# Optimization experiments

Hardware: AMD Instinct MI355X
Metric: run time of the kernel (lower is better)

The kernel has to match this reference:

```python
import jax, jax.numpy as jnp
import numpy as np

NUM_BINS = 16
D_MODEL = 128
TAIL_BOUND = 20.0
MIN_BIN_WIDTH = 1e-3
MIN_BIN_HEIGHT = 1e-3
MIN_DERIVATIVE = 1e-3
EPS = 1e-6


def setup_inputs() -> dict:
    key = jax.random.key(0)
    ks = jax.random.split(key, 10)
    B, S = 32, 8192
    sc = 0.05  # small init scale so spline logits stay moderate
    return {
        "inputs": jax.random.normal(ks[0], (B, S), dtype=jnp.float32),
        "conditioning": jax.random.normal(ks[1], (B, S, D_MODEL), dtype=jnp.float32),
        "Ww": jax.random.normal(ks[2], (NUM_BINS, D_MODEL), dtype=jnp.float32) * sc,
        "bw": jax.random.normal(ks[3], (NUM_BINS,), dtype=jnp.float32) * sc,
        "Wh": jax.random.normal(ks[4], (NUM_BINS, D_MODEL), dtype=jnp.float32) * sc,
        "bh": jax.random.normal(ks[5], (NUM_BINS,), dtype=jnp.float32) * sc,
        "Wd": jax.random.normal(ks[6], (NUM_BINS - 1, D_MODEL), dtype=jnp.float32) * sc,
        "bd": jax.random.normal(ks[7], (NUM_BINS - 1,), dtype=jnp.float32) * sc,
        "Wl": jax.random.normal(ks[8], (NUM_BINS, D_MODEL), dtype=jnp.float32) * sc,
        "bl": jax.random.normal(ks[9], (NUM_BINS,), dtype=jnp.float32) * sc,
    }


def _rational_linear_spline(x, uw, uh, ud, ul, left, right, bottom, top):
    nb = uw.shape[-1]
    # bin widths / cumulative widths
    w = MIN_BIN_WIDTH + (1.0 - MIN_BIN_WIDTH * nb) * jax.nn.softmax(uw, axis=-1)
    cw = jnp.concatenate([jnp.zeros_like(w[..., :1]), jnp.cumsum(w, axis=-1)], axis=-1)
    cw = (right - left) * cw + left
    cw = cw.at[..., 0].set(left).at[..., -1].set(right)
    w = cw[..., 1:] - cw[..., :-1]
    # derivatives (ud already padded to nb+1 by caller)
    d = MIN_DERIVATIVE + jax.nn.softplus(ud)
    # bin heights / cumulative heights
    h = MIN_BIN_HEIGHT + (1.0 - MIN_BIN_HEIGHT * nb) * jax.nn.softmax(uh, axis=-1)
    ch = jnp.concatenate([jnp.zeros_like(h[..., :1]), jnp.cumsum(h, axis=-1)], axis=-1)
    ch = (top - bottom) * ch + bottom
    ch = ch.at[..., 0].set(bottom).at[..., -1].set(top)
    h = ch[..., 1:] - ch[..., :-1]
    # searchsorted via sum of comparisons (as in source)
    locs = cw.at[..., -1].add(EPS)
    idx = jnp.sum((x[..., None] >= locs).astype(jnp.int32), axis=-1) - 1
    idx = jnp.clip(idx, 0, nb - 1)
    g = lambda t: jnp.take_along_axis(t, idx[..., None], axis=-1)[..., 0]
    in_cw = g(cw)
    in_bw = g(w)
    in_ch = g(ch)
    in_delta = g(h / w)
    dk = g(d)
    dk1 = g(d[..., 1:])
    in_h = g(h)
    lambdas = 0.95 * jax.nn.sigmoid(ul) + 0.025
    lam = g(lambdas)
    wa = 1.0
    wb = jnp.sqrt(dk / dk1) * wa
    wc = (lam * wa * dk + (1.0 - lam) * wb * dk1) / in_delta
    ya = in_ch
    yb = in_h + in_ch
    yc = ((1.0 - lam) * wa * ya + lam * wb * yb) / ((1.0 - lam) * wa + lam * wb)
    theta = (x - in_cw) / in_bw
    m = theta <= lam
    num = jnp.where(m, wa * ya * (lam - theta) + wc * yc * theta,
                    wc * yc * (1.0 - theta) + wb * yb * (theta - lam))
    den = jnp.where(m, wa * (lam - theta) + wc * theta,
                    wc * (1.0 - theta) + wb * (theta - lam))
    out = num / den
    deriv_num = jnp.where(m, wa * wc * lam * (yc - ya), wb * wc * (1.0 - lam) * (yb - yc)) / in_bw
    logabsdet = jnp.log(deriv_num) - 2.0 * jnp.log(jnp.abs(den))
    return out, logabsdet


def reference(inputs, conditioning, Ww, bw, Wh, bh, Wd, bd, Wl, bl):
    # parameter nets (module.forward): note the module normalizes here AND the
    # spline normalizes again -- replicate faithfully.
    uw = jax.nn.softmax(jnp.einsum('bsd,kd->bsk', conditioning, Ww) + bw, axis=-1)
    uh = jax.nn.softmax(jnp.einsum('bsd,kd->bsk', conditioning, Wh) + bh, axis=-1)
    ud = jax.nn.softplus(jnp.einsum('bsd,kd->bsk', conditioning, Wd) + bd)
    ul = jax.nn.sigmoid(jnp.einsum('bsd,kd->bsk', conditioning, Wl) + bl)
    # linear tails: pad derivatives with constant so boundary derivative == 1
    const = float(np.log(np.exp(1.0 - MIN_DERIVATIVE) - 1.0))
    edge = jnp.full(ud.shape[:-1] + (1,), const, dtype=ud.dtype)
    udp = jnp.concatenate([edge, ud, edge], axis=-1)  # [B,S,nb+1]
    tb = TAIL_BOUND
    inside = (inputs >= -tb) & (inputs <= tb)
    xc = jnp.clip(inputs, -tb, tb)
    s_out, s_lad = _rational_linear_spline(xc, uw, uh, udp, ul, -tb, tb, -tb, tb)
    outputs = jnp.where(inside, s_out, inputs)
    logabsdet = jnp.where(inside, s_lad, 0.0)
    return outputs, logabsdet
```

## Files before the change

### kernel.cpp

```cpp
#include <hip/hip_runtime.h>
#include <math.h>

#define NB 16
#define DM 128
#define BM 256
#define ZSTRIDE 68

typedef _Float16 half8  __attribute__((ext_vector_type(8)));
typedef _Float16 half4v __attribute__((ext_vector_type(4)));
typedef _Float16 half2v __attribute__((ext_vector_type(2)));
typedef __fp16   fp16x2 __attribute__((ext_vector_type(2)));
typedef float    f32x4  __attribute__((ext_vector_type(4)));

__device__ __forceinline__ float frcp_(float x) { return __builtin_amdgcn_rcpf(x); }
__device__ __forceinline__ float softplus_fast(float x) {
    return fmaxf(x, 0.0f) + __logf(1.0f + __expf(-fabsf(x)));
}
__device__ __forceinline__ float sigmoid_fast(float x) {
    return frcp_(1.0f + __expf(-x));
}
__device__ __forceinline__ void softmax16_m(float* z) {
    float m = z[0];
#pragma unroll
    for (int k = 1; k < NB; k++) m = fmaxf(m, z[k]);
    float s = 0.0f;
#pragma unroll
    for (int k = 0; k < NB; k++) { z[k] = __expf(z[k] - m); s += z[k]; }
    float r = frcp_(s);
#pragma unroll
    for (int k = 0; k < NB; k++) z[k] *= r;
}
__device__ __forceinline__ void softmax16_nm(float* z) {
    float s = 0.0f;
#pragma unroll
    for (int k = 0; k < NB; k++) { z[k] = __expf(z[k]); s += z[k]; }
    float r = frcp_(s);
#pragma unroll
    for (int k = 0; k < NB; k++) z[k] *= r;
}

__device__ __forceinline__ half2v pk_(float lo, float hi) {
    fp16x2 p = __builtin_amdgcn_cvt_pkrtz(lo, hi);
    return __builtin_bit_cast(half2v, p);
}
__device__ __forceinline__ half8 cvt8(float4 a0, float4 a1) {
    half2v p0 = pk_(a0.x, a0.y);
    half2v p1 = pk_(a0.z, a0.w);
    half2v p2 = pk_(a1.x, a1.y);
    half2v p3 = pk_(a1.z, a1.w);
    half8 f;
    f[0] = p0[0]; f[1] = p0[1]; f[2] = p1[0]; f[3] = p1[1];
    f[4] = p2[0]; f[5] = p2[1]; f[6] = p3[0]; f[7] = p3[1];
    return f;
}

#define LOADC(P, cr)                                    \
    P##0 = *(const float4*)((cr) + 0);                  \
    P##1 = *(const float4*)((cr) + 16);                 \
    P##2 = *(const float4*)((cr) + 32);                 \
    P##3 = *(const float4*)((cr) + 48);                 \
    P##4 = *(const float4*)((cr) + 64);                 \
    P##5 = *(const float4*)((cr) + 80);                 \
    P##6 = *(const float4*)((cr) + 96);                 \
    P##7 = *(const float4*)((cr) + 112);

#define CVTC(P)                                         \
    af0 = cvt8(P##0, P##1);                             \
    af1 = cvt8(P##2, P##3);                             \
    af2 = cvt8(P##4, P##5);                             \
    af3 = cvt8(P##6, P##7);

#define MFMA_S(af, s)                                                           \
    acc0 = __builtin_amdgcn_mfma_f32_16x16x32_f16(af, B0##s, acc0, 0, 0, 0);    \
    acc1 = __builtin_amdgcn_mfma_f32_16x16x32_f16(af, B1##s, acc1, 0, 0, 0);    \
    acc2 = __builtin_amdgcn_mfma_f32_16x16x32_f16(af, B2##s, acc2, 0, 0, 0);    \
    acc3 = __builtin_amdgcn_mfma_f32_16x16x32_f16(af, B3##s, acc3, 0, 0, 0);

#define STOREZ(c) {                                                             \
    _Float16* zpw = zbase + (size_t)((c) * 16) * ZSTRIDE;                       \
    _Pragma("unroll")                                                           \
    for (int r = 0; r < 4; r++) {                                               \
        half2v p0 = pk_(acc0[r], acc1[r]);                                      \
        half2v p1 = pk_(acc2[r], acc3[r]);                                      \
        half4v w; w[0] = p0[0]; w[1] = p0[1]; w[2] = p1[0]; w[3] = p1[1];       \
        *(half4v*)(zpw + (size_t)r * ZSTRIDE) = w;                              \
    } }

#define RESET_ACC  acc0 = zf4; acc1 = zf4; acc2 = zf4; acc3 = zf4;

#define GEMM_CHUNK(P, c)                                                        \
    CVTC(P)                                                                     \
    MFMA_S(af0, 0) MFMA_S(af1, 1) MFMA_S(af2, 2) MFMA_S(af3, 3)                 \
    STOREZ(c) RESET_ACC

#define STAGE_B(Wt, isWd, Q0, Q1, Q2, Q3) {                                     \
    const bool val = (!(isWd)) || (l15 < 15);                                   \
    const float* srcl = (Wt) + (size_t)(val ? l15 : 0) * DM + lg * 4;           \
    float4 q0 = *(const float4*)(srcl + 0),  q1 = *(const float4*)(srcl + 16);  \
    float4 q2 = *(const float4*)(srcl + 32), q3 = *(const float4*)(srcl + 48);  \
    float4 q4 = *(const float4*)(srcl + 64), q5 = *(const float4*)(srcl + 80);  \
    float4 q6 = *(const float4*)(srcl + 96), q7 = *(const float4*)(srcl + 112); \
    Q0 = val ? cvt8(q0, q1) : hz;                                               \
    Q1 = val ? cvt8(q2, q3) : hz;                                               \
    Q2 = val ? cvt8(q4, q5) : hz;                                               \
    Q3 = val ? cvt8(q6, q7) : hz; }

#define FENCE_LDS                                       \
    __builtin_amdgcn_sched_barrier(0);                  \
    asm volatile("s_waitcnt lgkmcnt(0)" ::: "memory");  \
    __builtin_amdgcn_sched_barrier(0);

#define EPILOGUE(xv, giv)                                                        \
  if ((giv) < (size_t)N) {                                                       \
    float zw[NB], zh[NB], zl[NB], zd[NB - 1];                                    \
    const half4v* zr4 = (const half4v*)&Z[(size_t)tid * ZSTRIDE];                \
    _Pragma("unroll")                                                            \
    for (int j = 0; j < NB; j++) {                                               \
        half4v v = zr4[j];                                                       \
        zw[j] = (float)v[0] + bw[j];                                             \
        zh[j] = (float)v[1] + bh[j];                                             \
        zl[j] = (float)v[2] + bl[j];                                             \
        if (j < NB - 1) zd[j] = (float)v[3] + bd[j];                             \
    }                                                                            \
    float xc = fminf(fmaxf((xv), -20.0f), 20.0f);                                \
    softmax16_m(zw);                                                             \
    softmax16_nm(zw);                                                            \
    const float scale = (1.0f - 1e-3f * NB);                                     \
    float cw[NB + 1];                                                            \
    cw[0] = -20.0f;                                                              \
    float cum = 0.0f;                                                            \
    _Pragma("unroll")                                                            \
    for (int k = 0; k < NB; k++) {                                               \
        cum += 1e-3f + scale * zw[k];                                            \
        cw[k + 1] = 40.0f * cum - 20.0f;                                         \
    }                                                                            \
    cw[NB] = 20.0f;                                                              \
    softmax16_m(zh);                                                             \
    softmax16_nm(zh);                                                            \
    float ch[NB + 1];                                                            \
    ch[0] = -20.0f;                                                              \
    cum = 0.0f;                                                                  \
    _Pragma("unroll")                                                            \
    for (int k = 0; k < NB; k++) {                                               \
        cum += 1e-3f + scale * zh[k];                                            \
        ch[k + 1] = 40.0f * cum - 20.0f;                                         \
    }                                                                            \
    ch[NB] = 20.0f;                                                              \
    float in_cw = cw[0], cw_hi = cw[1], in_ch = ch[0], ch_hi = ch[1];            \
    float zl_sel = zl[0], zd_lo = zd[0], zd_hi = zd[0];                          \
    _Pragma("unroll")                                                            \
    for (int k = 1; k < NB; k++) {                                               \
        bool take = (xc >= cw[k]);                                               \
        in_cw  = take ? cw[k]     : in_cw;                                       \
        cw_hi  = take ? cw[k + 1] : cw_hi;                                       \
        in_ch  = take ? ch[k]     : in_ch;                                       \
        ch_hi  = take ? ch[k + 1] : ch_hi;                                       \
        zl_sel = take ? zl[k]     : zl_sel;                                      \
        zd_lo  = take ? zd[k - 1] : zd_lo;                                       \
        zd_hi  = take ? zd[(k < NB - 1) ? k : NB - 2] : zd_hi;                   \
    }                                                                            \
    bool firstbin = (xc <  cw[1]);                                               \
    bool lastbin  = (xc >= cw[NB - 1]);                                          \
    float in_bw = cw_hi - in_cw;                                                 \
    float in_h  = ch_hi - in_ch;                                                 \
    float dk  = firstbin ? 1.0f : (1e-3f + softplus_fast(softplus_fast(zd_lo))); \
    float dk1 = lastbin  ? 1.0f : (1e-3f + softplus_fast(softplus_fast(zd_hi))); \
    float ul  = sigmoid_fast(zl_sel);                                            \
    float lam = 0.95f * sigmoid_fast(ul) + 0.025f;                               \
    float rbw = frcp_(in_bw);                                                    \
    float in_delta = in_h * rbw;                                                 \
    float wb = sqrtf(dk * frcp_(dk1));                                           \
    float wc = (lam * dk + (1.0f - lam) * wb * dk1) * frcp_(in_delta);           \
    float ya = in_ch;                                                            \
    float yb = in_h + in_ch;                                                     \
    float yc = ((1.0f - lam) * ya + lam * wb * yb) * frcp_((1.0f - lam) + lam * wb); \
    float theta = (xc - in_cw) * rbw;                                            \
    bool mlt = (theta <= lam);                                                   \
    float num = mlt ? (ya * (lam - theta) + wc * yc * theta)                     \
                    : (wc * yc * (1.0f - theta) + wb * yb * (theta - lam));      \
    float den = mlt ? ((lam - theta) + wc * theta)                               \
                    : (wc * (1.0f - theta) + wb * (theta - lam));                \
    float sout = num * frcp_(den);                                               \
    float dnum = (mlt ? (wc * lam * (yc - ya))                                   \
                      : (wb * wc * (1.0f - lam) * (yb - yc))) * rbw;             \
    float slad = __logf(dnum) - 2.0f * __logf(fabsf(den));                       \
    bool inside = ((xv) >= -20.0f) && ((xv) <= 20.0f);                           \
    out[(giv)] = inside ? sout : (xv);                                           \
    lad[(giv)] = inside ? slad : 0.0f;                                           \
  }

__global__ __launch_bounds__(256, 2) void spline_mfma(
    const float* __restrict__ xin, const float* __restrict__ cond,
    const float* __restrict__ Ww, const float* __restrict__ bw,
    const float* __restrict__ Wh, const float* __restrict__ bh,
    const float* __restrict__ Wd, const float* __restrict__ bd,
    const float* __restrict__ Wl, const float* __restrict__ bl,
    float* __restrict__ out, float* __restrict__ lad, int N)
{
    __shared__ __align__(16) _Float16 Z[BM * ZSTRIDE];

    const int tid  = threadIdx.x;
    const int wave = tid >> 6;
    const int lane = tid & 63;
    const int l15  = lane & 15;
    const int lg   = lane >> 4;

    const int nTiles = (N + BM - 1) / BM;
    const int t0 = (int)blockIdx.x;
    const int t1 = t0 + (int)gridDim.x;
    const bool hasT1 = (t1 < nTiles);

    half8 hz;
    hz[0]=hz[1]=hz[2]=hz[3]=hz[4]=hz[5]=hz[6]=hz[7] = (_Float16)0.0f;
    half8 B00, B01, B02, B03, B10, B11, B12, B13,
          B20, B21, B22, B23, B30, B31, B32, B33;
    STAGE_B(Ww, false, B00, B01, B02, B03)
    STAGE_B(Wh, false, B10, B11, B12, B13)
    STAGE_B(Wl, false, B20, B21, B22, B23)
    STAGE_B(Wd, true,  B30, B31, B32, B33)

    const size_t bRow0 = (size_t)t0 * BM;
    const size_t gi0 = bRow0 + tid;
    size_t g00 = bRow0 + (size_t)(wave * 64 + l15);
    size_t g01 = g00 + 16, g02 = g00 + 32, g03 = g00 + 48;
    if (g00 >= (size_t)N) g00 = (size_t)N - 1;
    if (g01 >= (size_t)N) g01 = (size_t)N - 1;
    if (g02 >= (size_t)N) g02 = (size_t)N - 1;
    if (g03 >= (size_t)N) g03 = (size_t)N - 1;

    float4 A0_0, A0_1, A0_2, A0_3, A0_4, A0_5, A0_6, A0_7;
    float4 A1_0, A1_1, A1_2, A1_3, A1_4, A1_5, A1_6, A1_7;
    float4 A2_0, A2_1, A2_2, A2_3, A2_4, A2_5, A2_6, A2_7;
    float4 A3_0, A3_1, A3_2, A3_3, A3_4, A3_5, A3_6, A3_7;
    LOADC(A0_, cond + g00 * DM + lg * 4)
    LOADC(A1_, cond + g01 * DM + lg * 4)
    LOADC(A2_, cond + g02 * DM + lg * 4)
    LOADC(A3_, cond + g03 * DM + lg * 4)
    float x0 = xin[gi0 < (size_t)N ? gi0 : 0];

    const f32x4 zf4 = {0.f, 0.f, 0.f, 0.f};
    f32x4 acc0 = zf4, acc1 = zf4, acc2 = zf4, acc3 = zf4;
    half8 af0, af1, af2, af3;
    _Float16* zbase = &Z[(size_t)(wave * 64 + lg * 4) * ZSTRIDE + l15 * 4];

    GEMM_CHUNK(A0_, 0)
    GEMM_CHUNK(A1_, 1)
    GEMM_CHUNK(A2_, 2)
    GEMM_CHUNK(A3_, 3)

    const size_t bRow1 = (size_t)t1 * BM;
    const size_t gi1 = bRow1 + tid;
    size_t g10 = bRow1 + (size_t)(wave * 64 + l15);
    size_t g11 = g10 + 16, g12 = g10 + 32, g13 = g10 + 48;
    if (g10 >= (size_t)N) g10 = (size_t)N - 1;
    if (g11 >= (size_t)N) g11 = (size_t)N - 1;
    if (g12 >= (size_t)N) g12 = (size_t)N - 1;
    if (g13 >= (size_t)N) g13 = (size_t)N - 1;
    float x1 = 0.0f;
    if (hasT1) {
        LOADC(A0_, cond + g10 * DM + lg * 4)
        LOADC(A1_, cond + g11 * DM + lg * 4)
        x1 = xin[gi1 < (size_t)N ? gi1 : 0];
    }

    FENCE_LDS
    EPILOGUE(x0, gi0)

    if (hasT1) {
        LOADC(A2_, cond + g12 * DM + lg * 4)
        LOADC(A3_, cond + g13 * DM + lg * 4)
        GEMM_CHUNK(A0_, 0)
        GEMM_CHUNK(A1_, 1)
        GEMM_CHUNK(A2_, 2)
        GEMM_CHUNK(A3_, 3)
        FENCE_LDS
        EPILOGUE(x1, gi1)
    }
}

extern "C" void kernel_launch(void* const* d_in, const int* in_sizes, int n_in,
                              void* d_out, int out_size, void* d_ws, size_t ws_size,
                              hipStream_t stream) {
    const float* xin  = (const float*)d_in[0];
    const float* cond = (const float*)d_in[1];
    const float* Ww   = (const float*)d_in[2];
    const float* bwp  = (const float*)d_in[3];
    const float* Wh   = (const float*)d_in[4];
    const float* bhp  = (const float*)d_in[5];
    const float* Wd   = (const float*)d_in[6];
    const float* bdp  = (const float*)d_in[7];
    const float* Wl   = (const float*)d_in[8];
    const float* blp  = (const float*)d_in[9];
    int N = in_sizes[0];
    float* out = (float*)d_out;
    float* lad = out + N;
    int nTiles = (N + BM - 1) / BM;
    int grid = (nTiles + 1) / 2;
    hipLaunchKernelGGL(spline_mfma, dim3(grid), dim3(256), 0, stream,
                       xin, cond, Ww, bwp, Wh, bhp, Wd, bdp, Wl, blp, out, lad, N);
}
```

Baseline: 35.29 us.

## Rotate three conditioning register buffers and compute spline knots inside the bin search

The prefetch schedule now rotates three A-register buffer sets instead of four. Loads for later chunks and the next tile are issued right after the buffer they reuse has been consumed by the MFMA chunk. The epilogue also computes cumulative widths and heights on the fly inside the bin-selection loop instead of materialising the cw/ch arrays. Together these lower register pressure, which could help occupancy, but they leave less prefetch distance before each chunk's data is needed.

```diff
diff --git a/kernel.cpp b/kernel.cpp
--- a/kernel.cpp
+++ b/kernel.cpp
@@ -109,6 +109,10 @@
     __builtin_amdgcn_sched_barrier(0);                  \
     asm volatile("s_waitcnt lgkmcnt(0)" ::: "memory");  \
     __builtin_amdgcn_sched_barrier(0);
+
+#define CPTR(t, c) (cond + ((((size_t)(t) * BM + (size_t)(wave * 64 + (c) * 16 + l15)) < (size_t)N) \
+                    ? ((size_t)(t) * BM + (size_t)(wave * 64 + (c) * 16 + l15))                     \
+                    : ((size_t)N - 1)) * DM + lg * 4)
 
 #define EPILOGUE(xv, giv)                                                        \
   if ((giv) < (size_t)N) {                                                       \
@@ -123,44 +127,35 @@
         if (j < NB - 1) zd[j] = (float)v[3] + bd[j];                             \
     }                                                                            \
     float xc = fminf(fmaxf((xv), -20.0f), 20.0f);                                \
-    softmax16_m(zw);                                                             \
-    softmax16_nm(zw);                                                            \
+    softmax16_m(zw); softmax16_nm(zw);                                           \
+    softmax16_m(zh); softmax16_nm(zh);                                           \
     const float scale = (1.0f - 1e-3f * NB);                                     \
-    float cw[NB + 1];                                                            \
-    cw[0] = -20.0f;                                                              \
-    float cum = 0.0f;                                                            \
-    _Pragma("unroll")                                                            \
-    for (int k = 0; k < NB; k++) {                                               \
-        cum += 1e-3f + scale * zw[k];                                            \
-        cw[k + 1] = 40.0f * cum - 20.0f;                                         \
-    }                                                                            \
-    cw[NB] = 20.0f;                                                              \
-    softmax16_m(zh);                                                             \
-    softmax16_nm(zh);                                                            \
-    float ch[NB + 1];                                                            \
-    ch[0] = -20.0f;                                                              \
-    cum = 0.0f;                                                                  \
-    _Pragma("unroll")                                                            \
-    for (int k = 0; k < NB; k++) {                                               \
-        cum += 1e-3f + scale * zh[k];                                            \
-        ch[k + 1] = 40.0f * cum - 20.0f;                                         \
-    }                                                                            \
-    ch[NB] = 20.0f;                                                              \
-    float in_cw = cw[0], cw_hi = cw[1], in_ch = ch[0], ch_hi = ch[1];            \
+    float cum_w = 1e-3f + scale * zw[0];                                         \
+    float cum_h = 1e-3f + scale * zh[0];                                         \
+    float cw_k1 = 40.0f * cum_w - 20.0f;                              \
+    float ch_k1 = 40.0f * cum_h - 20.0f;                                         \
+    const float cw1 = cw_k1;                                                     \
+    float in_cw = -20.0f, cw_hi = cw_k1, in_ch = -20.0f, ch_hi = ch_k1;          \
     float zl_sel = zl[0], zd_lo = zd[0], zd_hi = zd[0];                          \
+    bool lastbin = false;                                                        \
     _Pragma("unroll")                                                            \
     for (int k = 1; k < NB; k++) {                                               \
-        bool take = (xc >= cw[k]);                                               \
-        in_cw  = take ? cw[k]     : in_cw;                                       \
-        cw_hi  = take ? cw[k + 1] : cw_hi;                                       \
-        in_ch  = take ? ch[k]     : in_ch;                                       \
-        ch_hi  = take ? ch[k + 1] : ch_hi;                                       \
-        zl_sel = take ? zl[k]     : zl_sel;                                      \
+        cum_w += 1e-3f + scale * zw[k];                                          \
+        cum_h += 1e-3f + scale * zh[k];                                          \
+        float cw_k2 = (k == NB - 1) ? 20.0f : (40.0f * cum_w - 20.0f);           \
+        float ch_k2 = (k == NB - 1) ? 20.0f : (40.0f * cum_h - 20.0f);           \
+        bool take = (xc >= cw_k1);                              \
+        in_cw  = take ? cw_k1 : in_cw;                                           \
+        cw_hi  = take ? cw_k2 : cw_hi;                                           \
+        in_ch  = take ? ch_k1 : in_ch;                                           \
+        ch_hi  = take ? ch_k2 : ch_hi;                                           \
+        zl_sel = take ? zl[k] : zl_sel;                                          \
         zd_lo  = take ? zd[k - 1] : zd_lo;                                       \
         zd_hi  = take ? zd[(k < NB - 1) ? k : NB - 2] : zd_hi;                   \
+        if (k == NB - 1) lastbin = take;                                         \
+        cw_k1 = cw_k2; ch_k1 = ch_k2;                                            \
     }                                                                            \
-    bool firstbin = (xc <  cw[1]);                                               \
-    bool lastbin  = (xc >= cw[NB - 1]);                                          \
+    bool firstbin = (xc < cw1);                                                  \
     float in_bw = cw_hi - in_cw;                                                 \
     float in_h  = ch_hi - in_ch;                                                 \
     float dk  = firstbin ? 1.0f : (1e-3f + softplus_fast(softplus_fast(zd_lo))); \
@@ -219,23 +214,15 @@
     STAGE_B(Wl, false, B20, B21, B22, B23)
     STAGE_B(Wd, true,  B30, B31, B32, B33)
 
-    const size_t bRow0 = (size_t)t0 * BM;
-    const size_t gi0 = bRow0 + tid;
-    size_t g00 = bRow0 + (size_t)(wave * 64 + l15);
-    size_t g01 = g00 + 16, g02 = g00 + 32, g03 = g00 + 48;
-    if (g00 >= (size_t)N) g00 = (size_t)N - 1;
-    if (g01 >= (size_t)N) g01 = (size_t)N - 1;
-    if (g02 >= (size_t)N) g02 = (size_t)N - 1;
-    if (g03 >= (size_t)N) g03 = (size_t)N - 1;
+    const size_t gi0 = (size_t)t0 * BM + tid;
+    const size_t gi1 = (size_t)t1 * BM + tid;
 
     float4 A0_0, A0_1, A0_2, A0_3, A0_4, A0_5, A0_6, A0_7;
     float4 A1_0, A1_1, A1_2, A1_3, A1_4, A1_5, A1_6, A1_7;
     float4 A2_0, A2_1, A2_2, A2_3, A2_4, A2_5, A2_6, A2_7;
-    float4 A3_0, A3_1, A3_2, A3_3, A3_4, A3_5, A3_6, A3_7;
-    LOADC(A0_, cond + g00 * DM + lg * 4)
-    LOADC(A1_, cond + g01 * DM + lg * 4)
-    LOADC(A2_, cond + g02 * DM + lg * 4)
-    LOADC(A3_, cond + g03 * DM + lg * 4)
+    LOADC(A0_, CPTR(t0, 0))
+    LOADC(A1_, CPTR(t0, 1))
+    LOADC(A2_, CPTR(t0, 2))
     float x0 = xin[gi0 < (size_t)N ? gi0 : 0];
 
     const f32x4 zf4 = {0.f, 0.f, 0.f, 0.f};
@@ -244,22 +231,15 @@
     _Float16* zbase = &Z[(size_t)(wave * 64 + lg * 4) * ZSTRIDE + l15 * 4];
 
     GEMM_CHUNK(A0_, 0)
+    LOADC(A0_, CPTR(t0, 3))
     GEMM_CHUNK(A1_, 1)
+    float x1 = 0.0f;
+    if (hasT1) { LOADC(A1_, CPTR(t1, 0)) }
     GEMM_CHUNK(A2_, 2)
-    GEMM_CHUNK(A3_, 3)
-
-    const size_t bRow1 = (size_t)t1 * BM;
-    const size_t gi1 = bRow1 + tid;
-    size_t g10 = bRow1 + (size_t)(wave * 64 + l15);
-    size_t g11 = g10 + 16, g12 = g10 + 32, g13 = g10 + 48;
-    if (g10 >= (size_t)N) g10 = (size_t)N - 1;
-    if (g11 >= (size_t)N) g11 = (size_t)N - 1;
-    if (g12 >= (size_t)N) g12 = (size_t)N - 1;
-    if (g13 >= (size_t)N) g13 = (size_t)N - 1;
-    float x1 = 0.0f;
+    if (hasT1) { LOADC(A2_, CPTR(t1, 1)) }
+    GEMM_CHUNK(A0_, 3)
     if (hasT1) {
-        LOADC(A0_, cond + g10 * DM + lg * 4)
-        LOADC(A1_, cond + g11 * DM + lg * 4)
+        LOADC(A0_, CPTR(t1, 2))
         x1 = xin[gi1 < (size_t)N ? gi1 : 0];
     }
 
@@ -267,12 +247,11 @@
     EPILOGUE(x0, gi0)
 
     if (hasT1) {
-        LOADC(A2_, cond + g12 * DM + lg * 4)
-        LOADC(A3_, cond + g13 * DM + lg * 4)
-        GEMM_CHUNK(A0_, 0)
-        GEMM_CHUNK(A1_, 1)
-        GEMM_CHUNK(A2_, 2)
-        GEMM_CHUNK(A3_, 3)
+        GEMM_CHUNK(A1_, 0)
+        LOADC(A1_, CPTR(t1, 3))
+        GEMM_CHUNK(A2_, 1)
+        GEMM_CHUNK(A0_, 2)
+        GEMM_CHUNK(A1_, 3)
         FENCE_LDS
         EPILOGUE(x1, gi1)
     }
```

Measured after the change: 38.14 us. +8.1%, slower.

## Stage weights in LDS, process one tile per block, double-buffer loads

Applied to the files above, without the earlier changes.

Moves the converted fp16 weight fragments from per-thread registers into shared LDS, with each wave staging one weight matrix and then a block barrier. Each block now handles a single 256-row tile instead of two, and the conditioning loads use two rotating register buffers instead of four. Launch bounds rise to 3 blocks per CU. The aim is lower register pressure and higher occupancy, so that more memory requests are in flight. In exchange it adds LDS reads before every MFMA group, a __syncthreads, and repeats the weight staging in twice as many blocks.

```diff
diff --git a/kernel.cpp b/kernel.cpp
--- a/kernel.cpp
+++ b/kernel.cpp
@@ -70,11 +70,16 @@
     af2 = cvt8(P##4, P##5);                             \
     af3 = cvt8(P##6, P##7);
 
-#define MFMA_S(af, s)                                                           \
-    acc0 = __builtin_amdgcn_mfma_f32_16x16x32_f16(af, B0##s, acc0, 0, 0, 0);    \
-    acc1 = __builtin_amdgcn_mfma_f32_16x16x32_f16(af, B1##s, acc1, 0, 0, 0);    \
-    acc2 = __builtin_amdgcn_mfma_f32_16x16x32_f16(af, B2##s, acc2, 0, 0, 0);    \
-    acc3 = __builtin_amdgcn_mfma_f32_16x16x32_f16(af, B3##s, acc3, 0, 0, 0);
+#define MFMA_GRP(af, s) {                                                       \
+    const half8 bt0 = *(const half8*)(Blds + (((0*4+(s))*64 + lane) * 8));      \
+    const half8 bt1 = *(const half8*)(Blds + (((1*4+(s))*64 + lane) * 8));      \
+    const half8 bt2 = *(const half8*)(Blds + (((2*4+(s))*64 + lane) * 8));      \
+    const half8 bt3 = *(const half8*)(Blds + (((3*4+(s))*64 + lane) * 8));      \
+    acc0 = __builtin_amdgcn_mfma_f32_16x16x32_f16(af, bt0, acc0, 0, 0, 0);      \
+    acc1 = __builtin_amdgcn_mfma_f32_16x16x32_f16(af, bt1, acc1, 0, 0, 0);      \
+    acc2 = __builtin_amdgcn_mfma_f32_16x16x32_f16(af, bt2, acc2, 0, 0, 0);      \
+    acc3 = __builtin_amdgcn_mfma_f32_16x16x32_f16(af, bt3, acc3, 0, 0, 0);      \
+}
 
 #define STOREZ(c) {                                                             \
     _Float16* zpw = zbase + (size_t)((c) * 16) * ZSTRIDE;                       \
@@ -90,25 +95,34 @@
 
 #define GEMM_CHUNK(P, c)                                                        \
     CVTC(P)                                                                     \
-    MFMA_S(af0, 0) MFMA_S(af1, 1) MFMA_S(af2, 2) MFMA_S(af3, 3)                 \
+    MFMA_GRP(af0, 0) MFMA_GRP(af1, 1) MFMA_GRP(af2, 2) MFMA_GRP(af3, 3)         \
     STOREZ(c) RESET_ACC
 
-#define STAGE_B(Wt, isWd, Q0, Q1, Q2, Q3) {                                     \
+#define STAGE_B_LDS(Wt, isWd) {                                                 \
     const bool val = (!(isWd)) || (l15 < 15);                                   \
     const float* srcl = (Wt) + (size_t)(val ? l15 : 0) * DM + lg * 4;           \
     float4 q0 = *(const float4*)(srcl + 0),  q1 = *(const float4*)(srcl + 16);  \
     float4 q2 = *(const float4*)(srcl + 32), q3 = *(const float4*)(srcl + 48);  \
     float4 q4 = *(const float4*)(srcl + 64), q5 = *(const float4*)(srcl + 80);  \
     float4 q6 = *(const float4*)(srcl + 96), q7 = *(const float4*)(srcl + 112); \
-    Q0 = val ? cvt8(q0, q1) : hz;                                               \
-    Q1 = val ? cvt8(q2, q3) : hz;                                               \
-    Q2 = val ? cvt8(q4, q5) : hz;                                               \
-    Q3 = val ? cvt8(q6, q7) : hz; }
+    half8 Q0 = val ? cvt8(q0, q1) : hz;                                         \
+    half8 Q1 = val ? cvt8(q2, q3) : hz;                                         \
+    half8 Q2 = val ? cvt8(q4, q5) : hz;                                         \
+    half8 Q3 = val ? cvt8(q6, q7) : hz;                                         \
+    *(half8*)(Blds + (((wave*4+0)*64 + lane) * 8)) = Q0;                        \
+    *(half8*)(Blds + (((wave*4+1)*64 + lane) * 8)) = Q1;                        \
+    *(half8*)(Blds + (((wave*4+2)*64 + lane) * 8)) = Q2;                        \
+    *(half8*)(Blds + (((wave*4+3)*64 + lane) * 8)) = Q3;                        \
+}
 
 #define FENCE_LDS                                       \
     __builtin_amdgcn_sched_barrier(0);                  \
     asm volatile("s_waitcnt lgkmcnt(0)" ::: "memory");  \
     __builtin_amdgcn_sched_barrier(0);
+
+#define CPTR(c) (cond + (((bRow + (size_t)(wave * 64 + (c) * 16 + l15)) < (size_t)N) \
+                    ? (bRow + (size_t)(wave * 64 + (c) * 16 + l15))                  \
+                    : ((size_t)N - 1)) * DM + lg * 4)
 
 #define EPILOGUE(xv, giv)                                                        \
   if ((giv) < (size_t)N) {                                                       \
@@ -189,7 +203,7 @@
     lad[(giv)] = inside ? slad : 0.0f;                                           \
   }
 
-__global__ __launch_bounds__(256, 2) void spline_mfma(
+__global__ __launch_bounds__(256, 3) void spline_mfma(
     const float* __restrict__ xin, const float* __restrict__ cond,
     const float* __restrict__ Ww, const float* __restrict__ bw,
     const float* __restrict__ Wh, const float* __restrict__ bh,
@@ -198,6 +212,7 @@
     float* __restrict__ out, float* __restrict__ lad, int N)
 {
     __shared__ __align__(16) _Float16 Z[BM * ZSTRIDE];
+    __shared__ __align__(16) _Float16 Blds[16 * 64 * 8];
 
     const int tid  = threadIdx.x;
     const int wave = tid >> 6;
@@ -205,77 +220,38 @@
     const int l15  = lane & 15;
     const int lg   = lane >> 4;
 
-    const int nTiles = (N + BM - 1) / BM;
-    const int t0 = (int)blockIdx.x;
-    const int t1 = t0 + (int)gridDim.x;
-    const bool hasT1 = (t1 < nTiles);
+    const size_t bRow = (size_t)blockIdx.x * BM;
+    const size_t gi = bRow + tid;
 
     half8 hz;
     hz[0]=hz[1]=hz[2]=hz[3]=hz[4]=hz[5]=hz[6]=hz[7] = (_Float16)0.0f;
-    half8 B00, B01, B02, B03, B10, B11, B12, B13,
-          B20, B21, B22, B23, B30, B31, B32, B33;
-    STAGE_B(Ww, false, B00, B01, B02, B03)
-    STAGE_B(Wh, false, B10, B11, B12, B13)
-    STAGE_B(Wl, false, B20, B21, B22, B23)
-    STAGE_B(Wd, true,  B30, B31, B32, B33)
-
-    const size_t bRow0 = (size_t)t0 * BM;
-    const size_t gi0 = bRow0 + tid;
-    size_t g00 = bRow0 + (size_t)(wave * 64 + l15);
-    size_t g01 = g00 + 16, g02 = g00 + 32, g03 = g00 + 48;
-    if (g00 >= (size_t)N) g00 = (size_t)N - 1;
-    if (g01 >= (size_t)N) g01 = (size_t)N - 1;
-    if (g02 >= (size_t)N) g02 = (size_t)N - 1;
-    if (g03 >= (size_t)N) g03 = (size_t)N - 1;
-
-    float4 A0_0, A0_1, A0_2, A0_3, A0_4, A0_5, A0_6, A0_7;
-    float4 A1_0, A1_1, A1_2, A1_3, A1_4, A1_5, A1_6, A1_7;
-    float4 A2_0, A2_1, A2_2, A2_3, A2_4, A2_5, A2_6, A2_7;
-    float4 A3_0, A3_1, A3_2, A3_3, A3_4, A3_5, A3_6, A3_7;
-    LOADC(A0_, cond + g00 * DM + lg * 4)
-    LOADC(A1_, cond + g01 * DM + lg * 4)
-    LOADC(A2_, cond + g02 * DM + lg * 4)
-    LOADC(A3_, cond + g03 * DM + lg * 4)
-    float x0 = xin[gi0 < (size_t)N ? gi0 : 0];
+    {
+        const float* Wt = (wave == 0) ? Ww : (wave == 1) ? Wh : (wave == 2) ? Wl : Wd;
+        const bool isWd = (wave == 3);
+        STAGE_B_LDS(Wt, isWd)
+    }
+    __syncthreads();
+
+    float4 X0, X1, X2, X3, X4, X5, X6, X7;
+    float4 Y0, Y1, Y2, Y3, Y4, Y5, Y6, Y7;
+    LOADC(X, CPTR(0))
+    LOADC(Y, CPTR(1))
+    float x = xin[gi < (size_t)N ? gi : 0];
 
     const f32x4 zf4 = {0.f, 0.f, 0.f, 0.f};
     f32x4 acc0 = zf4, acc1 = zf4, acc2 = zf4, acc3 = zf4;
     half8 af0, af1, af2, af3;
     _Float16* zbase = &Z[(size_t)(wave * 64 + lg * 4) * ZSTRIDE + l15 * 4];
 
-    GEMM_CHUNK(A0_, 0)
-    GEMM_CHUNK(A1_, 1)
-    GEMM_CHUNK(A2_, 2)
-    GEMM_CHUNK(A3_, 3)
-
-    const size_t bRow1 = (size_t)t1 * BM;
-    const size_t gi1 = bRow1 + tid;
-    size_t g10 = bRow1 + (size_t)(wave * 64 + l15);
-    size_t g11 = g10 + 16, g12 = g10 + 32, g13 = g10 + 48;
-    if (g10 >= (size_t)N) g10 = (size_t)N - 1;
-    if (g11 >= (size_t)N) g11 = (size_t)N - 1;
-    if (g12 >= (size_t)N) g12 = (size_t)N - 1;
-    if (g13 >= (size_t)N) g13 = (size_t)N - 1;
-    float x1 = 0.0f;
-    if (hasT1) {
-        LOADC(A0_, cond + g10 * DM + lg * 4)
-        LOADC(A1_, cond + g11 * DM + lg * 4)
-        x1 = xin[gi1 < (size_t)N ? gi1 : 0];
-    }
+    GEMM_CHUNK(X, 0)
+    LOADC(X, CPTR(2))
+    GEMM_CHUNK(Y, 1)
+    LOADC(Y, CPTR(3))
+    GEMM_CHUNK(X, 2)
+    GEMM_CHUNK(Y, 3)
 
     FENCE_LDS
-    EPILOGUE(x0, gi0)
-
-    if (hasT1) {
-        LOADC(A2_, cond + g12 * DM + lg * 4)
-        LOADC(A3_, cond + g13 * DM + lg * 4)
-        GEMM_CHUNK(A0_, 0)
-        GEMM_CHUNK(A1_, 1)
-        GEMM_CHUNK(A2_, 2)
-        GEMM_CHUNK(A3_, 3)
-        FENCE_LDS
-        EPILOGUE(x1, gi1)
-    }
+    EPILOGUE(x, gi)
 }
 
 extern "C" void kernel_launch(void* const* d_in, const int* in_sizes, int n_in,
@@ -294,8 +270,7 @@
     int N = in_sizes[0];
     float* out = (float*)d_out;
     float* lad = out + N;
-    int nTiles = (N + BM - 1) / BM;
-    int grid = (nTiles + 1) / 2;
+    int grid = (N + BM - 1) / BM;
     hipLaunchKernelGGL(spline_mfma, dim3(grid), dim3(256), 0, stream,
                        xin, cond, Ww, bwp, Wh, bhp, Wd, bdp, Wl, blp, out, lad, N);
 }
```

Measured after the change: 33.84 us. 4.1% less time.

## Stage conditioning rows via global_load_lds with XOR swizzle, one tile per block

Applied to the files above, without the earlier changes.

Conditioning rows now go straight from global memory into LDS through global_load_lds, using an XOR-swizzled layout. Fragments are then read from LDS and converted to fp16 for MFMA, and loading of the next 16-row chunk overlaps with the MFMAs on the current one. The two-tile-per-block register-prefetch scheme is dropped in favour of one tile per block with twice the grid. The goal is to cut VGPR pressure and improve load coalescing, at the cost of 32KB of extra LDS per block, which may limit occupancy. It also removes the row clamping for partial tiles, so out-of-bounds reads are possible when N is not a multiple of 256.

```diff
diff --git a/kernel.cpp b/kernel.cpp
--- a/kernel.cpp
+++ b/kernel.cpp
@@ -54,21 +54,33 @@
     return f;
 }
 
-#define LOADC(P, cr)                                    \
-    P##0 = *(const float4*)((cr) + 0);                  \
-    P##1 = *(const float4*)((cr) + 16);                 \
-    P##2 = *(const float4*)((cr) + 32);                 \
-    P##3 = *(const float4*)((cr) + 48);                 \
-    P##4 = *(const float4*)((cr) + 64);                 \
-    P##5 = *(const float4*)((cr) + 80);                 \
-    P##6 = *(const float4*)((cr) + 96);                 \
-    P##7 = *(const float4*)((cr) + 112);
-
-#define CVTC(P)                                         \
-    af0 = cvt8(P##0, P##1);                             \
-    af1 = cvt8(P##2, P##3);                             \
-    af2 = cvt8(P##4, P##5);                             \
-    af3 = cvt8(P##6, P##7);
+#define GLL16(g, l)                                                             \
+    __builtin_amdgcn_global_load_lds(                                           \
+        (const __attribute__((address_space(1))) void*)(g),                     \
+        (__attribute__((address_space(3))) void*)(l), 16, 0, 0);
+
+#define ISSUE_A(c) {                                                            \
+    const char* gb_ = (const char*)(cond + (bRow + (size_t)(wave * 64 + (c) * 16)) * DM); \
+    _Pragma("unroll")                                                           \
+    for (int k_ = 0; k_ < 8; k_++) {                                            \
+        const unsigned r_ = 2u * k_ + lsel;                                     \
+        const char* ga_ = gb_ + (size_t)r_ * 512 + (cb32 ^ ((r_ & 7u) << 4));   \
+        GLL16(ga_, AstageW + k_ * 256)                                          \
+    } }
+
+#define RDFRAGS                                                                 \
+    fA = *(const float4*)(ab + ((128 * 0 + lgb) ^ swz));                        \
+    fB = *(const float4*)(ab + ((128 * 0 + 64 + lgb) ^ swz));                   \
+    af0 = cvt8(fA, fB);                                                         \
+    fA = *(const float4*)(ab + ((128 * 1 + lgb) ^ swz));                        \
+    fB = *(const float4*)(ab + ((128 * 1 + 64 + lgb) ^ swz));                   \
+    af1 = cvt8(fA, fB);                                                         \
+    fA = *(const float4*)(ab + ((128 * 2 + lgb) ^ swz));                        \
+    fB = *(const float4*)(ab + ((128 * 2 + 64 + lgb) ^ swz));                   \
+    af2 = cvt8(fA, fB);                                                         \
+    fA = *(const float4*)(ab + ((128 * 3 + lgb) ^ swz));                        \
+    fB = *(const float4*)(ab + ((128 * 3 + 64 + lgb) ^ swz));                   \
+    af3 = cvt8(fA, fB);
 
 #define MFMA_S(af, s)                                                           \
     acc0 = __builtin_amdgcn_mfma_f32_16x16x32_f16(af, B0##s, acc0, 0, 0, 0);    \
@@ -87,11 +99,6 @@
     } }
 
 #define RESET_ACC  acc0 = zf4; acc1 = zf4; acc2 = zf4; acc3 = zf4;
-
-#define GEMM_CHUNK(P, c)                                                        \
-    CVTC(P)                                                                     \
-    MFMA_S(af0, 0) MFMA_S(af1, 1) MFMA_S(af2, 2) MFMA_S(af3, 3)                 \
-    STOREZ(c) RESET_ACC
 
 #define STAGE_B(Wt, isWd, Q0, Q1, Q2, Q3) {                                     \
     const bool val = (!(isWd)) || (l15 < 15);                                   \
@@ -105,6 +112,10 @@
     Q2 = val ? cvt8(q4, q5) : hz;                                               \
     Q3 = val ? cvt8(q6, q7) : hz; }
 
+#define FENCE_VM                                        \
+    __builtin_amdgcn_sched_barrier(0);                  \
+    asm volatile("s_waitcnt vmcnt(0)" ::: "memory");    \
+    __builtin_amdgcn_sched_barrier(0);
 #define FENCE_LDS                                       \
     __builtin_amdgcn_sched_barrier(0);                  \
     asm volatile("s_waitcnt lgkmcnt(0)" ::: "memory");  \
@@ -198,17 +209,18 @@
     float* __restrict__ out, float* __restrict__ lad, int N)
 {
     __shared__ __align__(16) _Float16 Z[BM * ZSTRIDE];
+    __shared__ __align__(16) float Astage[4 * 2048];
 
     const int tid  = threadIdx.x;
     const int wave = tid >> 6;
     const int lane = tid & 63;
     const int l15  = lane & 15;
     const int lg   = lane >> 4;
-
-    const int nTiles = (N + BM - 1) / BM;
-    const int t0 = (int)blockIdx.x;
-    const int t1 = t0 + (int)gridDim.x;
-    const bool hasT1 = (t1 < nTiles);
+    const unsigned lsel = (unsigned)(lane >> 5);
+    const unsigned cb32 = (unsigned)((lane & 31) * 16);
+
+    const size_t bRow = (size_t)blockIdx.x * BM;
+    const size_t gi = bRow + tid;
 
     half8 hz;
     hz[0]=hz[1]=hz[2]=hz[3]=hz[4]=hz[5]=hz[6]=hz[7] = (_Float16)0.0f;
@@ -219,63 +231,45 @@
     STAGE_B(Wl, false, B20, B21, B22, B23)
     STAGE_B(Wd, true,  B30, B31, B32, B33)
 
-    const size_t bRow0 = (size_t)t0 * BM;
-    const size_t gi0 = bRow0 + tid;
-    size_t g00 = bRow0 + (size_t)(wave * 64 + l15);
-    size_t g01 = g00 + 16, g02 = g00 + 32, g03 = g00 + 48;
-    if (g00 >= (size_t)N) g00 = (size_t)N - 1;
-    if (g01 >= (size_t)N) g01 = (size_t)N - 1;
-    if (g02 >= (size_t)N) g02 = (size_t)N - 1;
-    if (g03 >= (size_t)N) g03 = (size_t)N - 1;
-
-    float4 A0_0, A0_1, A0_2, A0_3, A0_4, A0_5, A0_6, A0_7;
-    float4 A1_0, A1_1, A1_2, A1_3, A1_4, A1_5, A1_6, A1_7;
-    float4 A2_0, A2_1, A2_2, A2_3, A2_4, A2_5, A2_6, A2_7;
-    float4 A3_0, A3_1, A3_2, A3_3, A3_4, A3_5, A3_6, A3_7;
-    LOADC(A0_, cond + g00 * DM + lg * 4)
-    LOADC(A1_, cond + g01 * DM + lg * 4)
-    LOADC(A2_, cond + g02 * DM + lg * 4)
-    LOADC(A3_, cond + g03 * DM + lg * 4)
-    float x0 = xin[gi0 < (size_t)N ? gi0 : 0];
+    float* AstageW = Astage + wave * 2048;
+
+    ISSUE_A(0)
+    float x = xin[gi < (size_t)N ? gi : 0];
 
     const f32x4 zf4 = {0.f, 0.f, 0.f, 0.f};
     f32x4 acc0 = zf4, acc1 = zf4, acc2 = zf4, acc3 = zf4;
     half8 af0, af1, af2, af3;
+    float4 fA, fB;
     _Float16* zbase = &Z[(size_t)(wave * 64 + lg * 4) * ZSTRIDE + l15 * 4];
-
-    GEMM_CHUNK(A0_, 0)
-    GEMM_CHUNK(A1_, 1)
-    GEMM_CHUNK(A2_, 2)
-    GEMM_CHUNK(A3_, 3)
-
-    const size_t bRow1 = (size_t)t1 * BM;
-    const size_t gi1 = bRow1 + tid;
-    size_t g10 = bRow1 + (size_t)(wave * 64 + l15);
-    size_t g11 = g10 + 16, g12 = g10 + 32, g13 = g10 + 48;
-    if (g10 >= (size_t)N) g10 = (size_t)N - 1;
-    if (g11 >= (size_t)N) g11 = (size_t)N - 1;
-    if (g12 >= (size_t)N) g12 = (size_t)N - 1;
-    if (g13 >= (size_t)N) g13 = (size_t)N - 1;
-    float x1 = 0.0f;
-    if (hasT1) {
-        LOADC(A0_, cond + g10 * DM + lg * 4)
-        LOADC(A1_, cond + g11 * DM + lg * 4)
-        x1 = xin[gi1 < (size_t)N ? gi1 : 0];
-    }
-
-    FENCE_LDS
-    EPILOGUE(x0, gi0)
-
-    if (hasT1) {
-        LOADC(A2_, cond + g12 * DM + lg * 4)
-        LOADC(A3_, cond + g13 * DM + lg * 4)
-        GEMM_CHUNK(A0_, 0)
-        GEMM_CHUNK(A1_, 1)
-        GEMM_CHUNK(A2_, 2)
-        GEMM_CHUNK(A3_, 3)
-        FENCE_LDS
-        EPILOGUE(x1, gi1)
-    }
+    const char* ab = (const char*)AstageW + l15 * 512;
+    const unsigned swz = (unsigned)((l15 & 7) << 4);
+    const unsigned lgb = (unsigned)(lg * 16);
+
+    FENCE_VM
+    RDFRAGS
+    FENCE_LDS
+    ISSUE_A(1)
+    MFMA_S(af0, 0) MFMA_S(af1, 1) MFMA_S(af2, 2) MFMA_S(af3, 3)
+    STOREZ(0) RESET_ACC
+    FENCE_VM
+    RDFRAGS
+    FENCE_LDS
+    ISSUE_A(2)
+    MFMA_S(af0, 0) MFMA_S(af1, 1) MFMA_S(af2, 2) MFMA_S(af3, 3)
+    STOREZ(1) RESET_ACC
+    FENCE_VM
+    RDFRAGS
+    FENCE_LDS
+    ISSUE_A(3)
+    MFMA_S(af0, 0) MFMA_S(af1, 1) MFMA_S(af2, 2) MFMA_S(af3, 3)
+    STOREZ(2) RESET_ACC
+    FENCE_VM
+    RDFRAGS
+    MFMA_S(af0, 0) MFMA_S(af1, 1) MFMA_S(af2, 2) MFMA_S(af3, 3)
+    STOREZ(3)
+
+    FENCE_LDS
+    EPILOGUE(x, gi)
 }
 
 extern "C" void kernel_launch(void* const* d_in, const int* in_sizes, int n_in,
@@ -294,8 +288,7 @@
     int N = in_sizes[0];
     float* out = (float*)d_out;
     float* lad = out + N;
-    int nTiles = (N + BM - 1) / BM;
-    int grid = (nTiles + 1) / 2;
+    int grid = (N + BM - 1) / BM;
     hipLaunchKernelGGL(spline_mfma, dim3(grid), dim3(256), 0, stream,
                        xin, cond, Ww, bwp, Wh, bhp, Wd, bdp, Wl, blp, out, lad, N);
 }
```

Result: slower. 39.35 us (+11.5%).
